# Optimization experiments

Measured on AMD Instinct MI355X. Metric: run time of the kernel, lower is better.

## Reference

```python
import jax, jax.numpy as jnp
import numpy as np

HIDDEN = 128
EDGE = 64
EPS = 1e-5

def setup_inputs() -> dict:
    key = jax.random.key(0)
    ks = jax.random.split(key, 12)
    B, N, D = 8, 256, HIDDEN
    h = jax.random.normal(ks[0], (B, N, D), dtype=jnp.float32)
    edge_feats = jax.random.normal(ks[1], (B, N, N, 3), dtype=jnp.float32)
    adj_mask = jax.random.bernoulli(ks[2], 0.5, (B, N, N))
    s = lambda fan_in: 1.0 / np.sqrt(fan_in)
    W1 = jax.random.uniform(ks[3], (D + 3, EDGE), minval=-s(D + 3), maxval=s(D + 3))
    b1 = jnp.zeros((EDGE,), jnp.float32)
    W2 = jax.random.uniform(ks[4], (EDGE, D), minval=-s(EDGE), maxval=s(EDGE))
    b2 = jnp.zeros((D,), jnp.float32)
    U1 = jax.random.uniform(ks[5], (3 * D, D), minval=-s(3 * D), maxval=s(3 * D))
    b3 = jnp.zeros((D,), jnp.float32)
    U2 = jax.random.uniform(ks[6], (D, D), minval=-s(D), maxval=s(D))
    b4 = jnp.zeros((D,), jnp.float32)
    gamma = jnp.ones((D,), jnp.float32)
    beta = jnp.zeros((D,), jnp.float32)
    return {"h": h, "edge_feats": edge_feats, "adj_mask": adj_mask,
            "W1": W1, "b1": b1, "W2": W2, "b2": b2,
            "U1": U1, "b3": b3, "U2": U2, "b4": b4,
            "gamma": gamma, "beta": beta}

def reference(h, edge_feats, adj_mask, W1, b1, W2, b2, U1, b3, U2, b4, gamma, beta):
    B, N, D = h.shape
    # NOTE: torch does h.unsqueeze(2).expand(B,N,N,D): h_j[b,i,j,:] = h[b,i,:]
    h_j = jnp.broadcast_to(h[:, :, None, :], (B, N, N, D))
    gate_in = jnp.concatenate([h_j, edge_feats], axis=-1)          # (B,N,N,D+3)
    gates = jax.nn.sigmoid(jax.nn.relu(gate_in @ W1 + b1) @ W2 + b2)  # (B,N,N,D)
    mask_f = adj_mask.astype(h.dtype)[..., None]                    # (B,N,N,1)
    messages = gates * h_j * mask_f
    neighbor_count = jnp.clip(jnp.sum(mask_f, axis=2), 1.0)         # (B,N,1)
    agg_mean = jnp.sum(messages, axis=2) / neighbor_count           # (B,N,D)
    msgs_max = jnp.where(adj_mask[..., None], messages, -jnp.inf)
    agg_max = jnp.max(msgs_max, axis=2)
    agg_max = jnp.where(jnp.isinf(agg_max), 0.0, agg_max)
    upd_in = jnp.concatenate([h, agg_mean, agg_max], axis=-1)       # (B,N,3D)
    upd = jax.nn.relu(upd_in @ U1 + b3) @ U2 + b4
    x = h + upd
    mu = jnp.mean(x, axis=-1, keepdims=True)
    var = jnp.var(x, axis=-1, keepdims=True)
    return (x - mu) * jax.lax.rsqrt(var + EPS) * gamma + beta
```

## Files before the change

kernel.cpp:

```cpp
#include <hip/hip_runtime.h>
#include <hip/hip_bf16.h>
#include <math.h>

#define NN 256
#define DD 128
#define EE 64
#define TPAD 72
#define APAD 392
#define RPAD 136

typedef __attribute__((ext_vector_type(8))) short short8;
typedef __attribute__((ext_vector_type(4))) float f32x4;

static __device__ __forceinline__ unsigned short f2bf(float f) {
    __hip_bfloat16 b = __float2bfloat16(f);
    return *reinterpret_cast<unsigned short*>(&b);
}

static __device__ __forceinline__ short8 ldb(const float* __restrict__ B, int kbase, int d) {
    unsigned short tmp[8];
    #pragma unroll
    for (int j = 0; j < 8; ++j) tmp[j] = f2bf(B[(kbase + j) * DD + d]);
    return *(const short8*)tmp;
}

__global__ __launch_bounds__(256, 6)
void ecgc_gate(const float* __restrict__ h_g,
               const float* __restrict__ ef_g,
               const int*   __restrict__ mask_g,
               const float* __restrict__ W1_g,
               const float* __restrict__ b1_g,
               const float* __restrict__ W2_g,
               const float* __restrict__ b2_g,
               float*       __restrict__ ws)
{
    const int bi   = blockIdx.x;
    const int t    = threadIdx.x;
    const int lane = t & 63;
    const int w    = t >> 6;
    const int m16  = lane & 15;
    const int quad = lane >> 4;

    __shared__ __align__(16) unsigned short shT[64 * TPAD];
    __shared__ __align__(16) float sh_ef[NN * 4];
    __shared__ __align__(16) float sh_base[EE];
    __shared__ __align__(16) float sh_w1e[3 * EE];
    __shared__ float sh_h[DD];
    __shared__ float sh_basep[4 * EE];
    __shared__ int   sh_jlist[NN], sh_wcnt[4], sh_cnt;

    if (t < DD) sh_h[t] = h_g[bi * DD + t];
    if (t < 192) sh_w1e[t] = W1_g[(DD + (t >> 6)) * EE + (t & 63)];
    {
        const float* efr = ef_g + (size_t)bi * NN * 3;
        sh_ef[t * 4 + 0] = efr[t * 3 + 0];
        sh_ef[t * 4 + 1] = efr[t * 3 + 1];
        sh_ef[t * 4 + 2] = efr[t * 3 + 2];
        sh_ef[t * 4 + 3] = 0.f;
    }
    const int mk = (mask_g[bi * NN + t] != 0) ? 1 : 0;
    const unsigned long long bal = __ballot(mk);
    if (lane == 0) sh_wcnt[w] = __popcll(bal);
    const int pre = __popcll(bal & ((1ull << lane) - 1ull));

    const int dstripe = w * 32;
    short8 bfrag[2][2];
    float  nb2[2];
    #pragma unroll
    for (int dt = 0; dt < 2; ++dt) {
        const int d = dstripe + 16 * dt + m16;
        nb2[dt] = b2_g[d];
        #pragma unroll
        for (int kh = 0; kh < 2; ++kh)
            bfrag[dt][kh] = ldb(W2_g, kh * 32 + quad * 8, d);
    }
    __syncthreads();

    {
        int wbase = 0;
        for (int ww = 0; ww < w; ++ww) wbase += sh_wcnt[ww];
        if (mk) sh_jlist[wbase + pre] = t;
        if (t == 0) sh_cnt = sh_wcnt[0] + sh_wcnt[1] + sh_wcnt[2] + sh_wcnt[3];
    }
    {
        const int e = t & 63, dgrp = t >> 6;
        float acc = 0.f;
        #pragma unroll 4
        for (int d = dgrp * 32; d < dgrp * 32 + 32; ++d)
            acc = fmaf(sh_h[d], W1_g[d * EE + e], acc);
        sh_basep[dgrp * EE + e] = acc;
    }
    __syncthreads();
    if (t < EE)
        sh_base[t] = b1_g[t] + sh_basep[t] + sh_basep[EE + t] +
                     sh_basep[2 * EE + t] + sh_basep[3 * EE + t];
    __syncthreads();

    const int cnt = sh_cnt;
    const int nch = (cnt + 63) >> 6;

    float sumv[2] = {0.f, 0.f};
    float mxv[2]  = {-__builtin_inff(), -__builtin_inff()};
    float mnv[2]  = { __builtin_inff(),  __builtin_inff()};

    for (int ch = 0; ch < nch; ++ch) {
        {
            const int row = t >> 2, e0 = (t & 3) * 16;
            const int js  = ch * 64 + row;
            const int ok  = (js < cnt);
            float e0f = 0.f, e1f = 0.f, e2f = 0.f;
            if (ok) {
                const float4 efv = *(const float4*)&sh_ef[sh_jlist[js] * 4];
                e0f = efv.x; e1f = efv.y; e2f = efv.z;
            }
            unsigned short pk[16];
            #pragma unroll
            for (int vb = 0; vb < 4; ++vb) {
                const float4 bs = *(const float4*)&sh_base[e0 + vb * 4];
                const float4 w0 = *(const float4*)&sh_w1e[e0 + vb * 4];
                const float4 w1 = *(const float4*)&sh_w1e[64 + e0 + vb * 4];
                const float4 w2 = *(const float4*)&sh_w1e[128 + e0 + vb * 4];
                const float bsx[4] = {bs.x, bs.y, bs.z, bs.w};
                const float w0x[4] = {w0.x, w0.y, w0.z, w0.w};
                const float w1x[4] = {w1.x, w1.y, w1.z, w1.w};
                const float w2x[4] = {w2.x, w2.y, w2.z, w2.w};
                #pragma unroll
                for (int v = 0; v < 4; ++v) {
                    float tv = 0.f;
                    if (ok)
                        tv = fmaxf(fmaf(e0f, w0x[v],
                                   fmaf(e1f, w1x[v],
                                   fmaf(e2f, w2x[v], bsx[v]))), 0.f);
                    pk[vb * 4 + v] = f2bf(tv);
                }
            }
            *(short8*)&shT[row * TPAD + e0]     = *(const short8*)&pk[0];
            *(short8*)&shT[row * TPAD + e0 + 8] = *(const short8*)&pk[8];
        }
        __syncthreads();

        const int rem = min(64, cnt - ch * 64);
        const int jtn = (rem + 15) >> 4;
        for (int jt = 0; jt < jtn; ++jt) {
            const short8 a0 = *(const short8*)&shT[(jt * 16 + m16) * TPAD + quad * 8];
            const short8 a1 = *(const short8*)&shT[(jt * 16 + m16) * TPAD + 32 + quad * 8];
            const int jbase = ch * 64 + jt * 16 + quad * 4;
            #pragma unroll
            for (int dt = 0; dt < 2; ++dt) {
                f32x4 acc = {0.f, 0.f, 0.f, 0.f};
                acc = __builtin_amdgcn_mfma_f32_16x16x32_bf16(a0, bfrag[dt][0], acc, 0, 0, 0);
                acc = __builtin_amdgcn_mfma_f32_16x16x32_bf16(a1, bfrag[dt][1], acc, 0, 0, 0);
                #pragma unroll
                for (int r = 0; r < 4; ++r) {
                    const float g = __fdividef(1.f, 1.f + __expf(-(acc[r] + nb2[dt])));
                    if (jbase + r < cnt) {
                        sumv[dt] += g;
                        mxv[dt]  = fmaxf(mxv[dt], g);
                        mnv[dt]  = fminf(mnv[dt], g);
                    }
                }
            }
        }
        __syncthreads();
    }

    #pragma unroll
    for (int dt = 0; dt < 2; ++dt) {
        float s = sumv[dt], M = mxv[dt], mn = mnv[dt];
        s += __shfl_xor(s, 16, 64);  s += __shfl_xor(s, 32, 64);
        M  = fmaxf(M,  __shfl_xor(M, 16, 64));  M  = fmaxf(M,  __shfl_xor(M, 32, 64));
        mn = fminf(mn, __shfl_xor(mn, 16, 64)); mn = fminf(mn, __shfl_xor(mn, 32, 64));
        if (quad == 0) {
            const int d  = dstripe + 16 * dt + m16;
            const float hd = sh_h[d];
            float mean = 0.f, amax = 0.f;
            if (cnt > 0) {
                mean = hd * s * __fdividef(1.f, (float)cnt);
                amax = (hd >= 0.f) ? hd * M : hd * mn;
            }
            ws[bi * 256 + d]       = mean;
            ws[bi * 256 + 128 + d] = amax;
        }
    }
}

__global__ __launch_bounds__(256, 2)
void ecgc_upd(const float* __restrict__ h_g,
              const float* __restrict__ ws,
              const float* __restrict__ U1_g,
              const float* __restrict__ b3_g,
              const float* __restrict__ U2_g,
              const float* __restrict__ b4_g,
              const float* __restrict__ gam_g,
              const float* __restrict__ bet_g,
              float*       __restrict__ out_g)
{
    const int bi0  = blockIdx.x * 16;
    const int t    = threadIdx.x;
    const int lane = t & 63;
    const int w    = t >> 6;
    const int m16  = lane & 15;
    const int quad = lane >> 4;

    __shared__ __align__(16) unsigned short shA[16 * APAD];
    __shared__ __align__(16) unsigned short rbuf[16 * RPAD];
    __shared__ float sh_s[4 * 16], sh_s2[4 * 16], sh_mu[16], sh_rs[16];

    {
        const int row = t >> 4, q = t & 15;
        const float* hrow = h_g + (size_t)(bi0 + row) * DD;
        const float* wrow = ws  + (size_t)(bi0 + row) * 256;
        unsigned short tmp[24];
        #pragma unroll
        for (int c = 0; c < 24; ++c) {
            const int col = q * 24 + c;
            float v;
            if (col < 128)      v = hrow[col];
            else if (col < 256) v = wrow[col - 128];
            else                v = wrow[col - 256 + 128];
            tmp[c] = f2bf(v);
        }
        #pragma unroll
        for (int s8 = 0; s8 < 3; ++s8)
            *(short8*)&shA[row * APAD + q * 24 + s8 * 8] = *(const short8*)&tmp[s8 * 8];
    }
    __syncthreads();

    const int dstripe = w * 32;

    f32x4 acc[2] = {{0.f, 0.f, 0.f, 0.f}, {0.f, 0.f, 0.f, 0.f}};
    for (int kk = 0; kk < 12; ++kk) {
        const short8 a0 = *(const short8*)&shA[m16 * APAD + kk * 32 + quad * 8];
        #pragma unroll
        for (int dt = 0; dt < 2; ++dt) {
            const short8 b = ldb(U1_g, kk * 32 + quad * 8, dstripe + dt * 16 + m16);
            acc[dt] = __builtin_amdgcn_mfma_f32_16x16x32_bf16(a0, b, acc[dt], 0, 0, 0);
        }
    }

    #pragma unroll
    for (int dt = 0; dt < 2; ++dt) {
        const int d = dstripe + dt * 16 + m16;
        const float bb = b3_g[d];
        #pragma unroll
        for (int r = 0; r < 4; ++r) {
            const int ro = quad * 4 + r;
            rbuf[ro * RPAD + d] = f2bf(fmaxf(acc[dt][r] + bb, 0.f));
        }
    }
    __syncthreads();

    f32x4 acc2[2] = {{0.f, 0.f, 0.f, 0.f}, {0.f, 0.f, 0.f, 0.f}};
    for (int kk = 0; kk < 4; ++kk) {
        const short8 a0 = *(const short8*)&rbuf[m16 * RPAD + kk * 32 + quad * 8];
        #pragma unroll
        for (int dt = 0; dt < 2; ++dt) {
            const short8 b = ldb(U2_g, kk * 32 + quad * 8, dstripe + dt * 16 + m16);
            acc2[dt] = __builtin_amdgcn_mfma_f32_16x16x32_bf16(a0, b, acc2[dt], 0, 0, 0);
        }
    }

    float xv[2][4];
    #pragma unroll
    for (int dt = 0; dt < 2; ++dt) {
        const int d = dstripe + dt * 16 + m16;
        const float bb = b4_g[d];
        #pragma unroll
        for (int r = 0; r < 4; ++r) {
            const int ro = quad * 4 + r;
            xv[dt][r] = h_g[(size_t)(bi0 + ro) * DD + d] + acc2[dt][r] + bb;
        }
    }

    #pragma unroll
    for (int r = 0; r < 4; ++r) {
        float s  = xv[0][r] + xv[1][r];
        float s2 = xv[0][r] * xv[0][r] + xv[1][r] * xv[1][r];
        #pragma unroll
        for (int off = 1; off < 16; off <<= 1) {
            s  += __shfl_xor(s,  off, 64);
            s2 += __shfl_xor(s2, off, 64);
        }
        if (m16 == 0) {
            const int ro = quad * 4 + r;
            sh_s[w * 16 + ro]  = s;
            sh_s2[w * 16 + ro] = s2;
        }
    }
    __syncthreads();
    if (t < 16) {
        const float S  = sh_s[t]  + sh_s[16 + t]  + sh_s[32 + t]  + sh_s[48 + t];
        const float S2 = sh_s2[t] + sh_s2[16 + t] + sh_s2[32 + t] + sh_s2[48 + t];
        const float mu  = S * (1.f / 128.f);
        const float var = S2 * (1.f / 128.f) - mu * mu;
        sh_mu[t] = mu;
        sh_rs[t] = rsqrtf(var + 1e-5f);
    }
    __syncthreads();

    #pragma unroll
    for (int dt = 0; dt < 2; ++dt) {
        const int d = dstripe + dt * 16 + m16;
        const float ga = gam_g[d], be = bet_g[d];
        #pragma unroll
        for (int r = 0; r < 4; ++r) {
            const int ro = quad * 4 + r;
            out_g[(size_t)(bi0 + ro) * DD + d] =
                (xv[dt][r] - sh_mu[ro]) * sh_rs[ro] * ga + be;
        }
    }
}

extern "C" void kernel_launch(void* const* d_in, const int* in_sizes, int n_in,
                              void* d_out, int out_size, void* d_ws, size_t ws_size,
                              hipStream_t stream) {
    float* ws = (float*)d_ws;
    ecgc_gate<<<8 * NN, 256, 0, stream>>>(
        (const float*)d_in[0],
        (const float*)d_in[1],
        (const int*)d_in[2],
        (const float*)d_in[3],
        (const float*)d_in[4],
        (const float*)d_in[5],
        (const float*)d_in[6],
        ws);
    ecgc_upd<<<(8 * NN) / 16, 256, 0, stream>>>(
        (const float*)d_in[0],
        ws,
        (const float*)d_in[7],
        (const float*)d_in[8],
        (const float*)d_in[9],
        (const float*)d_in[10],
        (const float*)d_in[11],
        (const float*)d_in[12],
        (float*)d_out);
}
```

Baseline: 125.5 us.

## Build gate MLP A-fragments in registers and pre-transpose U weights to bf16

The gate kernel no longer stages the ReLU hidden layer in shared memory. Each lane computes its own bf16 MFMA A-fragment directly from per-lane copies of the base and edge weights, which removes the chunk loop and its two barriers per chunk. Sigmoid is applied once to the reduced max and min logits instead of per element for those reductions, and b2/b3/b4 are folded into the accumulator initialisation. The gate blocks also transpose U1 and U2 to bf16 in workspace, so the update kernel can load B fragments as vectors instead of strided fp32 gathers. The risks are more registers (the occupancy hint drops from 6 to 4) and a dependency on the first kernel writing the transposed weights.

```diff
diff --git a/kernel.cpp b/kernel.cpp
--- a/kernel.cpp
+++ b/kernel.cpp
@@ -5,7 +5,6 @@
 #define NN 256
 #define DD 128
 #define EE 64
-#define TPAD 72
 #define APAD 392
 #define RPAD 136
 
@@ -24,7 +23,11 @@
     return *(const short8*)tmp;
 }
 
-__global__ __launch_bounds__(256, 6)
+static __device__ __forceinline__ float sigm(float l) {
+    return __fdividef(1.f, 1.f + __expf(-l));
+}
+
+__global__ __launch_bounds__(256, 4)
 void ecgc_gate(const float* __restrict__ h_g,
                const float* __restrict__ ef_g,
                const int*   __restrict__ mask_g,
@@ -32,7 +35,11 @@
                const float* __restrict__ b1_g,
                const float* __restrict__ W2_g,
                const float* __restrict__ b2_g,
-               float*       __restrict__ ws)
+               const float* __restrict__ U1_g,
+               const float* __restrict__ U2_g,
+               float*          __restrict__ aggf,
+               unsigned short* __restrict__ u1t,
+               unsigned short* __restrict__ u2t)
 {
     const int bi   = blockIdx.x;
     const int t    = threadIdx.x;
@@ -41,27 +48,46 @@
     const int m16  = lane & 15;
     const int quad = lane >> 4;
 
-    __shared__ __align__(16) unsigned short shT[64 * TPAD];
-    __shared__ __align__(16) float sh_ef[NN * 4];
-    __shared__ __align__(16) float sh_base[EE];
-    __shared__ __align__(16) float sh_w1e[3 * EE];
-    __shared__ float sh_h[DD];
+    __shared__ __align__(16) float sh_ef4[NN * 4];
+    __shared__ __align__(16) float sh_q4[EE * 4];
     __shared__ float sh_basep[4 * EE];
+    __shared__ float sh_w1e[3 * EE];
     __shared__ int   sh_jlist[NN], sh_wcnt[4], sh_cnt;
 
-    if (t < DD) sh_h[t] = h_g[bi * DD + t];
-    if (t < 192) sh_w1e[t] = W1_g[(DD + (t >> 6)) * EE + (t & 63)];
+    if (t < 32) {
+        const int flat = bi * 32 + t;
+        if (flat < 384 * DD) {
+            const int d = flat / 384, k = flat - d * 384;
+            u1t[flat] = f2bf(U1_g[k * DD + d]);
+        } else {
+            const int f2 = flat - 384 * DD;
+            const int d = f2 >> 7, k = f2 & 127;
+            u2t[f2] = f2bf(U2_g[k * DD + d]);
+        }
+    }
+
     {
         const float* efr = ef_g + (size_t)bi * NN * 3;
-        sh_ef[t * 4 + 0] = efr[t * 3 + 0];
-        sh_ef[t * 4 + 1] = efr[t * 3 + 1];
-        sh_ef[t * 4 + 2] = efr[t * 3 + 2];
-        sh_ef[t * 4 + 3] = 0.f;
-    }
+        sh_ef4[t * 4 + 0] = efr[t * 3 + 0];
+        sh_ef4[t * 4 + 1] = efr[t * 3 + 1];
+        sh_ef4[t * 4 + 2] = efr[t * 3 + 2];
+        sh_ef4[t * 4 + 3] = 0.f;
+    }
+    if (t < 192) sh_w1e[t] = W1_g[(DD + (t >> 6)) * EE + (t & 63)];
+
     const int mk = (mask_g[bi * NN + t] != 0) ? 1 : 0;
     const unsigned long long bal = __ballot(mk);
     if (lane == 0) sh_wcnt[w] = __popcll(bal);
     const int pre = __popcll(bal & ((1ull << lane) - 1ull));
+
+    {
+        const int e = t & 63;
+        float acc = 0.f;
+        #pragma unroll 8
+        for (int d = w * 32; d < w * 32 + 32; ++d)
+            acc = fmaf(h_g[bi * DD + d], W1_g[d * EE + e], acc);
+        sh_basep[w * EE + e] = acc;
+    }
 
     const int dstripe = w * 32;
     short8 bfrag[2][2];
@@ -82,114 +108,104 @@
         if (mk) sh_jlist[wbase + pre] = t;
         if (t == 0) sh_cnt = sh_wcnt[0] + sh_wcnt[1] + sh_wcnt[2] + sh_wcnt[3];
     }
-    {
-        const int e = t & 63, dgrp = t >> 6;
-        float acc = 0.f;
-        #pragma unroll 4
-        for (int d = dgrp * 32; d < dgrp * 32 + 32; ++d)
-            acc = fmaf(sh_h[d], W1_g[d * EE + e], acc);
-        sh_basep[dgrp * EE + e] = acc;
-    }
-    __syncthreads();
-    if (t < EE)
-        sh_base[t] = b1_g[t] + sh_basep[t] + sh_basep[EE + t] +
-                     sh_basep[2 * EE + t] + sh_basep[3 * EE + t];
-    __syncthreads();
+    if (t < EE) {
+        const float base = b1_g[t] + sh_basep[t] + sh_basep[EE + t] +
+                           sh_basep[2 * EE + t] + sh_basep[3 * EE + t];
+        sh_q4[t * 4 + 0] = base;
+        sh_q4[t * 4 + 1] = sh_w1e[t];
+        sh_q4[t * 4 + 2] = sh_w1e[EE + t];
+        sh_q4[t * 4 + 3] = sh_w1e[2 * EE + t];
+    }
+    __syncthreads();
+
+    f32x4 qa[8], qb[8];
+    #pragma unroll
+    for (int jj = 0; jj < 8; ++jj) {
+        qa[jj] = *(const f32x4*)&sh_q4[(quad * 8 + jj) * 4];
+        qb[jj] = *(const f32x4*)&sh_q4[(32 + quad * 8 + jj) * 4];
+    }
 
     const int cnt = sh_cnt;
-    const int nch = (cnt + 63) >> 6;
-
-    float sumv[2] = {0.f, 0.f};
-    float mxv[2]  = {-__builtin_inff(), -__builtin_inff()};
-    float mnv[2]  = { __builtin_inff(),  __builtin_inff()};
-
-    for (int ch = 0; ch < nch; ++ch) {
-        {
-            const int row = t >> 2, e0 = (t & 3) * 16;
-            const int js  = ch * 64 + row;
-            const int ok  = (js < cnt);
-            float e0f = 0.f, e1f = 0.f, e2f = 0.f;
-            if (ok) {
-                const float4 efv = *(const float4*)&sh_ef[sh_jlist[js] * 4];
-                e0f = efv.x; e1f = efv.y; e2f = efv.z;
-            }
-            unsigned short pk[16];
-            #pragma unroll
-            for (int vb = 0; vb < 4; ++vb) {
-                const float4 bs = *(const float4*)&sh_base[e0 + vb * 4];
-                const float4 w0 = *(const float4*)&sh_w1e[e0 + vb * 4];
-                const float4 w1 = *(const float4*)&sh_w1e[64 + e0 + vb * 4];
-                const float4 w2 = *(const float4*)&sh_w1e[128 + e0 + vb * 4];
-                const float bsx[4] = {bs.x, bs.y, bs.z, bs.w};
-                const float w0x[4] = {w0.x, w0.y, w0.z, w0.w};
-                const float w1x[4] = {w1.x, w1.y, w1.z, w1.w};
-                const float w2x[4] = {w2.x, w2.y, w2.z, w2.w};
+    const int njt = (cnt + 15) >> 4;
+
+    float sum2[2] = {0.f, 0.f};
+    float mxl[2]  = {-3.0e38f, -3.0e38f};
+    float mnl[2]  = { 3.0e38f,  3.0e38f};
+
+    for (int jt = 0; jt < njt; ++jt) {
+        const int row = jt * 16 + m16;
+        int jl = sh_jlist[row];
+        jl = (row < cnt) ? jl : 0;
+        const float4 efv = *(const float4*)&sh_ef4[jl * 4];
+
+        union { short8 s; __hip_bfloat162 h2[4]; } ua, ub;
+        #pragma unroll
+        for (int p = 0; p < 4; ++p) {
+            const f32x4 qa0 = qa[2 * p], qa1 = qa[2 * p + 1];
+            const f32x4 qb0 = qb[2 * p], qb1 = qb[2 * p + 1];
+            float2 va, vb;
+            va.x = fmaxf(fmaf(efv.z, qa0[3], fmaf(efv.y, qa0[2], fmaf(efv.x, qa0[1], qa0[0]))), 0.f);
+            va.y = fmaxf(fmaf(efv.z, qa1[3], fmaf(efv.y, qa1[2], fmaf(efv.x, qa1[1], qa1[0]))), 0.f);
+            vb.x = fmaxf(fmaf(efv.z, qb0[3], fmaf(efv.y, qb0[2], fmaf(efv.x, qb0[1], qb0[0]))), 0.f);
+            vb.y = fmaxf(fmaf(efv.z, qb1[3], fmaf(efv.y, qb1[2], fmaf(efv.x, qb1[1], qb1[0]))), 0.f);
+            ua.h2[p] = __float22bfloat162_rn(va);
+            ub.h2[p] = __float22bfloat162_rn(vb);
+        }
+
+        const bool tail = (jt == njt - 1) && (cnt & 15);
+        #pragma unroll
+        for (int dt = 0; dt < 2; ++dt) {
+            f32x4 acc = {nb2[dt], nb2[dt], nb2[dt], nb2[dt]};
+            acc = __builtin_amdgcn_mfma_f32_16x16x32_bf16(ua.s, bfrag[dt][0], acc, 0, 0, 0);
+            acc = __builtin_amdgcn_mfma_f32_16x16x32_bf16(ub.s, bfrag[dt][1], acc, 0, 0, 0);
+            if (!tail) {
                 #pragma unroll
-                for (int v = 0; v < 4; ++v) {
-                    float tv = 0.f;
-                    if (ok)
-                        tv = fmaxf(fmaf(e0f, w0x[v],
-                                   fmaf(e1f, w1x[v],
-                                   fmaf(e2f, w2x[v], bsx[v]))), 0.f);
-                    pk[vb * 4 + v] = f2bf(tv);
+                for (int r = 0; r < 4; ++r) {
+                    const float l = acc[r];
+                    mxl[dt] = fmaxf(mxl[dt], l);
+                    mnl[dt] = fminf(mnl[dt], l);
+                    sum2[dt] += sigm(l);
+                }
+            } else {
+                #pragma unroll
+                for (int r = 0; r < 4; ++r) {
+                    const bool v = (jt * 16 + quad * 4 + r) < cnt;
+                    const float lx = v ? acc[r] : -3.0e38f;
+                    const float ln = v ? acc[r] :  3.0e38f;
+                    mxl[dt] = fmaxf(mxl[dt], lx);
+                    mnl[dt] = fminf(mnl[dt], ln);
+                    sum2[dt] += sigm(lx);
                 }
             }
-            *(short8*)&shT[row * TPAD + e0]     = *(const short8*)&pk[0];
-            *(short8*)&shT[row * TPAD + e0 + 8] = *(const short8*)&pk[8];
-        }
-        __syncthreads();
-
-        const int rem = min(64, cnt - ch * 64);
-        const int jtn = (rem + 15) >> 4;
-        for (int jt = 0; jt < jtn; ++jt) {
-            const short8 a0 = *(const short8*)&shT[(jt * 16 + m16) * TPAD + quad * 8];
-            const short8 a1 = *(const short8*)&shT[(jt * 16 + m16) * TPAD + 32 + quad * 8];
-            const int jbase = ch * 64 + jt * 16 + quad * 4;
-            #pragma unroll
-            for (int dt = 0; dt < 2; ++dt) {
-                f32x4 acc = {0.f, 0.f, 0.f, 0.f};
-                acc = __builtin_amdgcn_mfma_f32_16x16x32_bf16(a0, bfrag[dt][0], acc, 0, 0, 0);
-                acc = __builtin_amdgcn_mfma_f32_16x16x32_bf16(a1, bfrag[dt][1], acc, 0, 0, 0);
-                #pragma unroll
-                for (int r = 0; r < 4; ++r) {
-                    const float g = __fdividef(1.f, 1.f + __expf(-(acc[r] + nb2[dt])));
-                    if (jbase + r < cnt) {
-                        sumv[dt] += g;
-                        mxv[dt]  = fmaxf(mxv[dt], g);
-                        mnv[dt]  = fminf(mnv[dt], g);
-                    }
-                }
-            }
-        }
-        __syncthreads();
-    }
-
-    #pragma unroll
-    for (int dt = 0; dt < 2; ++dt) {
-        float s = sumv[dt], M = mxv[dt], mn = mnv[dt];
+        }
+    }
+
+    #pragma unroll
+    for (int dt = 0; dt < 2; ++dt) {
+        float s = sum2[dt], M = mxl[dt], m2 = mnl[dt];
         s += __shfl_xor(s, 16, 64);  s += __shfl_xor(s, 32, 64);
         M  = fmaxf(M,  __shfl_xor(M, 16, 64));  M  = fmaxf(M,  __shfl_xor(M, 32, 64));
-        mn = fminf(mn, __shfl_xor(mn, 16, 64)); mn = fminf(mn, __shfl_xor(mn, 32, 64));
+        m2 = fminf(m2, __shfl_xor(m2, 16, 64)); m2 = fminf(m2, __shfl_xor(m2, 32, 64));
         if (quad == 0) {
-            const int d  = dstripe + 16 * dt + m16;
-            const float hd = sh_h[d];
+            const int d = dstripe + 16 * dt + m16;
+            const float hd = h_g[bi * DD + d];
             float mean = 0.f, amax = 0.f;
             if (cnt > 0) {
                 mean = hd * s * __fdividef(1.f, (float)cnt);
-                amax = (hd >= 0.f) ? hd * M : hd * mn;
+                amax = (hd >= 0.f) ? hd * sigm(M) : hd * sigm(m2);
             }
-            ws[bi * 256 + d]       = mean;
-            ws[bi * 256 + 128 + d] = amax;
+            aggf[bi * 256 + d]       = mean;
+            aggf[bi * 256 + 128 + d] = amax;
         }
     }
 }
 
 __global__ __launch_bounds__(256, 2)
 void ecgc_upd(const float* __restrict__ h_g,
-              const float* __restrict__ ws,
-              const float* __restrict__ U1_g,
+              const float* __restrict__ aggf,
+              const unsigned short* __restrict__ u1t,
+              const unsigned short* __restrict__ u2t,
               const float* __restrict__ b3_g,
-              const float* __restrict__ U2_g,
               const float* __restrict__ b4_g,
               const float* __restrict__ gam_g,
               const float* __restrict__ bet_g,
@@ -208,8 +224,8 @@
 
     {
         const int row = t >> 4, q = t & 15;
-        const float* hrow = h_g + (size_t)(bi0 + row) * DD;
-        const float* wrow = ws  + (size_t)(bi0 + row) * 256;
+        const float* hrow = h_g  + (size_t)(bi0 + row) * DD;
+        const float* wrow = aggf + (size_t)(bi0 + row) * 256;
         unsigned short tmp[24];
         #pragma unroll
         for (int c = 0; c < 24; ++c) {
@@ -228,12 +244,18 @@
 
     const int dstripe = w * 32;
 
-    f32x4 acc[2] = {{0.f, 0.f, 0.f, 0.f}, {0.f, 0.f, 0.f, 0.f}};
+    f32x4 acc[2];
+    #pragma unroll
+    for (int dt = 0; dt < 2; ++dt) {
+        const float bb = b3_g[dstripe + dt * 16 + m16];
+        acc[dt] = (f32x4){bb, bb, bb, bb};
+    }
     for (int kk = 0; kk < 12; ++kk) {
         const short8 a0 = *(const short8*)&shA[m16 * APAD + kk * 32 + quad * 8];
         #pragma unroll
         for (int dt = 0; dt < 2; ++dt) {
-            const short8 b = ldb(U1_g, kk * 32 + quad * 8, dstripe + dt * 16 + m16);
+            const int d = dstripe + dt * 16 + m16;
+            const short8 b = *(const short8*)&u1t[(size_t)d * 384 + kk * 32 + quad * 8];
             acc[dt] = __builtin_amdgcn_mfma_f32_16x16x32_bf16(a0, b, acc[dt], 0, 0, 0);
         }
     }
@@ -241,21 +263,26 @@
     #pragma unroll
     for (int dt = 0; dt < 2; ++dt) {
         const int d = dstripe + dt * 16 + m16;
-        const float bb = b3_g[d];
         #pragma unroll
         for (int r = 0; r < 4; ++r) {
             const int ro = quad * 4 + r;
-            rbuf[ro * RPAD + d] = f2bf(fmaxf(acc[dt][r] + bb, 0.f));
-        }
-    }
-    __syncthreads();
-
-    f32x4 acc2[2] = {{0.f, 0.f, 0.f, 0.f}, {0.f, 0.f, 0.f, 0.f}};
+            rbuf[ro * RPAD + d] = f2bf(fmaxf(acc[dt][r], 0.f));
+        }
+    }
+    __syncthreads();
+
+    f32x4 acc2[2];
+    #pragma unroll
+    for (int dt = 0; dt < 2; ++dt) {
+        const float bb = b4_g[dstripe + dt * 16 + m16];
+        acc2[dt] = (f32x4){bb, bb, bb, bb};
+    }
     for (int kk = 0; kk < 4; ++kk) {
         const short8 a0 = *(const short8*)&rbuf[m16 * RPAD + kk * 32 + quad * 8];
         #pragma unroll
         for (int dt = 0; dt < 2; ++dt) {
-            const short8 b = ldb(U2_g, kk * 32 + quad * 8, dstripe + dt * 16 + m16);
+            const int d = dstripe + dt * 16 + m16;
+            const short8 b = *(const short8*)&u2t[(size_t)d * 128 + kk * 32 + quad * 8];
             acc2[dt] = __builtin_amdgcn_mfma_f32_16x16x32_bf16(a0, b, acc2[dt], 0, 0, 0);
         }
     }
@@ -264,11 +291,10 @@
     #pragma unroll
     for (int dt = 0; dt < 2; ++dt) {
         const int d = dstripe + dt * 16 + m16;
-        const float bb = b4_g[d];
         #pragma unroll
         for (int r = 0; r < 4; ++r) {
             const int ro = quad * 4 + r;
-            xv[dt][r] = h_g[(size_t)(bi0 + ro) * DD + d] + acc2[dt][r] + bb;
+            xv[dt][r] = h_g[(size_t)(bi0 + ro) * DD + d] + acc2[dt][r];
         }
     }
 
@@ -314,7 +340,9 @@
 extern "C" void kernel_launch(void* const* d_in, const int* in_sizes, int n_in,
                               void* d_out, int out_size, void* d_ws, size_t ws_size,
                               hipStream_t stream) {
-    float* ws = (float*)d_ws;
+    float* aggf = (float*)d_ws;
+    unsigned short* u1t = (unsigned short*)((char*)d_ws + (size_t)2048 * 256 * 4);
+    unsigned short* u2t = u1t + 384 * DD;
     ecgc_gate<<<8 * NN, 256, 0, stream>>>(
         (const float*)d_in[0],
         (const float*)d_in[1],
@@ -323,13 +351,13 @@
         (const float*)d_in[4],
         (const float*)d_in[5],
         (const float*)d_in[6],
-        ws);
+        (const float*)d_in[7],
+        (const float*)d_in[9],
+        aggf, u1t, u2t);
     ecgc_upd<<<(8 * NN) / 16, 256, 0, stream>>>(
         (const float*)d_in[0],
-        ws,
-        (const float*)d_in[7],
+        aggf, u1t, u2t,
         (const float*)d_in[8],
-        (const float*)d_in[9],
         (const float*)d_in[10],
         (const float*)d_in[11],
         (const float*)d_in[12],
```

Measured after the change: 122.6 us. 2.3% less time.
